# Performance work log

Measured on AMD Instinct MI355X. Metric: run time of the kernel, lower is better.

Reference implementation:

```python
import jax, jax.numpy as jnp
import numpy as np

B, T, D, H = 128, 512, 256, 512


def setup_inputs() -> dict:
    key = jax.random.key(0)
    k1, k2, k3 = jax.random.split(key, 3)
    x = jax.random.normal(k1, (B, T, D), dtype=jnp.float32)
    Wx = jax.random.normal(k2, (D, 4 * H), dtype=jnp.float32) * 0.05
    Wh = jax.random.normal(k3, (H, 4 * H), dtype=jnp.float32) * 0.05
    b = jnp.zeros((4 * H,), dtype=jnp.float32)
    return {"x": x, "Wx": Wx, "Wh": Wh, "b": b}


def reference(x, Wx, Wh, b):
    # DynamicRNN: transpose [B,T,D]->[T,B,D], unroll LSTM cell per timestep,
    # stack outputs, transpose back, return (outputs, final_state).
    xs = jnp.transpose(x, (1, 0, 2))  # [T, B, D]
    Bn = x.shape[0]
    Hn = Wh.shape[0]
    h0 = jnp.zeros((Bn, Hn), dtype=x.dtype)
    c0 = jnp.zeros((Bn, Hn), dtype=x.dtype)

    # Precompute input-side projection for all timesteps (same math, batched).
    zx = jnp.einsum('tbd,dg->tbg', xs, Wx) + b  # [T, B, 4H]

    def step(carry, zx_t):
        h, c = carry
        z = zx_t + h @ Wh  # [B, 4H]
        i, f, g, o = jnp.split(z, 4, axis=-1)
        i = jax.nn.sigmoid(i)
        f = jax.nn.sigmoid(f)
        g = jnp.tanh(g)
        o = jax.nn.sigmoid(o)
        c_new = f * c + i * g
        h_new = o * jnp.tanh(c_new)
        return (h_new, c_new), h_new

    (hT, cT), ys = jax.lax.scan(step, (h0, c0), zx)  # ys: [T, B, H]
    outputs = jnp.transpose(ys, (1, 0, 2))  # [B, T, H]
    return (outputs, hT, cT)
```

## Files before the change

kernel.cpp:

```cpp
#include <hip/hip_runtime.h>
#include <hip/hip_bf16.h>


#define B_   128
#define T_   512
#define D_   256
#define H_   512
#define G4_  2048
#define NBLK 128
#define KH   16
#define KX   8
#define XROW 264

typedef __attribute__((ext_vector_type(8))) short short8;
typedef __attribute__((ext_vector_type(4))) short short4v;
typedef __attribute__((ext_vector_type(4))) float float4v;
typedef __attribute__((ext_vector_type(4))) int   int4v;

__device__ inline unsigned short f2bf_bits(float f) {
    union { float f; unsigned u; } v; v.f = f;
    unsigned r = (v.u + 0x7FFFu + ((v.u >> 16) & 1u)) >> 16;
    return (unsigned short)r;
}

__device__ inline float sigmoid_fast(float x) {
    return 1.f / (1.f + __expf(-x));
}

__device__ inline float tanh_fast(float x) {
    float a = fabsf(x);
    float e = __expf(-2.f * a);
    float r = (1.f - e) / (1.f + e);
    return copysignf(r, x);
}

__device__ inline short4v pack_bf4(float4v v) {
    short4v o;
    o[0] = (short)f2bf_bits(v[0]);
    o[1] = (short)f2bf_bits(v[1]);
    o[2] = (short)f2bf_bits(v[2]);
    o[3] = (short)f2bf_bits(v[3]);
    return o;
}

union HAu { int4v i4; short8 s8; };

__global__ __launch_bounds__(512, 2) void lstm_persistent(
    const float* __restrict__ x, const float* __restrict__ Wx,
    const float* __restrict__ Wh, const float* __restrict__ bias,
    float* __restrict__ out, unsigned short* __restrict__ hbuf,
    unsigned int* __restrict__ flags)
{
    const int tid  = threadIdx.x;
    const int lane = tid & 63;
    const int wave = tid >> 6;
    const int ms   = wave & 3;
    const int nt   = wave >> 2;
    const int ct   = blockIdx.x & 63;
    const int bt   = blockIdx.x >> 6;
    const int jh0  = ct * 8;

    __shared__ float zls[64 * 33];
    __shared__ float cls[64 * 8];
    __shared__ float bls[32];
    __shared__ unsigned short xls[2][64 * XROW];

    for (int i = tid; i < 64 * 8; i += 512) cls[i] = 0.f;
    if (tid < 32) bls[tid] = bias[(tid >> 3) * 512 + jh0 + (tid & 7)];

    const int l15 = lane & 15;
    const int l4  = lane >> 4;
    const int ncol = nt * 16 + l15;
    const int col  = (ncol >> 3) * 512 + jh0 + (ncol & 7);
    short8 wfrag[KX + KH];
#pragma unroll
    for (int ks = 0; ks < KX + KH; ++ks) {
        short8 w;
#pragma unroll
        for (int j = 0; j < 8; ++j) {
            int k = ks * 32 + l4 * 8 + j;
            float v = (k < D_) ? Wx[(size_t)k * G4_ + col]
                               : Wh[(size_t)(k - D_) * G4_ + col];
            w[j] = (short)f2bf_bits(v);
        }
        wfrag[ks] = w;
    }

    const int srow = tid >> 5;
    const int scol = (tid & 31) * 4;
    const float* xbase = x + (size_t)(bt * 64) * (T_ * D_);

    const int mrow = ms * 16 + l15;
    const int gb_a = bt * 64 + mrow;

    const int bl = tid >> 3, ug = tid & 7;
    const int gb_g = bt * 64 + bl;

    unsigned int* myflag = flags + bt * 64 + lane;

    short4v rxp[8];
#pragma unroll
    for (int r = 0; r < 4; ++r) {
        const float* xp = xbase + (size_t)(r * 16 + srow) * (T_ * D_);
        int row = r * 16 + srow;
        *(short4v*)(&xls[0][row * XROW + scol]) =
            pack_bf4(*(const float4v*)(xp + scol));
        *(short4v*)(&xls[0][row * XROW + scol + 128]) =
            pack_bf4(*(const float4v*)(xp + scol + 128));
    }
    __syncthreads();
    float4v accx = {0.f, 0.f, 0.f, 0.f};
#pragma unroll
    for (int ks = 0; ks < KX; ++ks) {
        short8 a = *(const short8*)(&xls[0][mrow * XROW + ks * 32 + l4 * 8]);
        accx = __builtin_amdgcn_mfma_f32_16x16x32_bf16(a, wfrag[ks], accx, 0, 0, 0);
    }
#pragma unroll
    for (int r = 0; r < 4; ++r) {
        const float* xp = xbase + (size_t)(r * 16 + srow) * (T_ * D_) + D_;
        rxp[r * 2]     = pack_bf4(*(const float4v*)(xp + scol));
        rxp[r * 2 + 1] = pack_bf4(*(const float4v*)(xp + scol + 128));
    }

    int cur = 0;
    for (int t = 0; t < T_; ++t) {
        if (t + 1 < T_) {
            unsigned short* xb = xls[(t + 1) & 1];
#pragma unroll
            for (int r = 0; r < 4; ++r) {
                int row = r * 16 + srow;
                *(short4v*)(xb + row * XROW + scol)       = rxp[r * 2];
                *(short4v*)(xb + row * XROW + scol + 128) = rxp[r * 2 + 1];
            }
        }

        if (t) {
            unsigned tgt = (unsigned)t;
            while (true) {
                unsigned f = __hip_atomic_load(myflag, __ATOMIC_RELAXED,
                                               __HIP_MEMORY_SCOPE_AGENT);
                if (__all((int)(f >= tgt))) break;
            }
        }

        HAu ha[KH];
        {
            const unsigned short* hb0 =
                hbuf + ((size_t)(cur * 64 + l4) * 128 + gb_a) * 8;
#pragma unroll
            for (int ks = 0; ks < KH; ++ks) {
                const unsigned short* ap = hb0 + (size_t)ks * (4 * 128 * 8);
                asm volatile("global_load_dwordx4 %0, %1, off sc0 sc1"
                             : "=v"(ha[ks].i4) : "v"(ap));
            }
        }

        float4v a0 = accx;
        float4v a1 = {0.f, 0.f, 0.f, 0.f};
        asm volatile("s_waitcnt vmcnt(8)" ::: "memory");
        __builtin_amdgcn_sched_barrier(0);
#pragma unroll
        for (int ks = 0; ks < 8; ++ks)
            a0 = __builtin_amdgcn_mfma_f32_16x16x32_bf16(
                     ha[ks].s8, wfrag[KX + ks], a0, 0, 0, 0);
        asm volatile("s_waitcnt vmcnt(0)" ::: "memory");
        __builtin_amdgcn_sched_barrier(0);
#pragma unroll
        for (int ks = 8; ks < KH; ++ks)
            a1 = __builtin_amdgcn_mfma_f32_16x16x32_bf16(
                     ha[ks].s8, wfrag[KX + ks], a1, 0, 0, 0);
#pragma unroll
        for (int r = 0; r < 4; ++r) {
            int row = ms * 16 + l4 * 4 + r;
            zls[row * 33 + nt * 16 + l15] = a0[r] + a1[r];
        }
        __syncthreads();

        {
            float zi = zls[bl * 33 + ug]      + bls[ug];
            float zf = zls[bl * 33 + 8 + ug]  + bls[8 + ug];
            float zg = zls[bl * 33 + 16 + ug] + bls[16 + ug];
            float zo = zls[bl * 33 + 24 + ug] + bls[24 + ug];
            float ig = sigmoid_fast(zi);
            float fg = sigmoid_fast(zf);
            float gg = tanh_fast(zg);
            float og = sigmoid_fast(zo);
            float cold = cls[bl * 8 + ug];
            float cnew = fg * cold + ig * gg;
            float hnew = og * tanh_fast(cnew);
            cls[bl * 8 + ug] = cnew;
            unsigned hv = (unsigned)f2bf_bits(hnew);
            unsigned short* hp = hbuf
                + ((size_t)(((t + 1) & 1) * 64 + ct) * 128 + gb_g) * 8 + ug;
            asm volatile("global_store_short %0, %1, off sc0 sc1"
                         :: "v"(hp), "v"(hv) : "memory");
            out[(size_t)gb_g * (T_ * H_) + (size_t)t * H_ + jh0 + ug] = hnew;
            if (t == T_ - 1) {
                const size_t BTH = (size_t)B_ * T_ * H_;
                out[BTH + (size_t)gb_g * H_ + jh0 + ug] = hnew;
                out[BTH + (size_t)B_ * H_ + (size_t)gb_g * H_ + jh0 + ug] = cnew;
            }
        }
        asm volatile("s_waitcnt vmcnt(0)" ::: "memory");
        __syncthreads();

        if (tid == 0)
            __hip_atomic_store(flags + bt * 64 + ct, (unsigned)(t + 1),
                               __ATOMIC_RELAXED, __HIP_MEMORY_SCOPE_AGENT);

        float4v nacc = {0.f, 0.f, 0.f, 0.f};
        if (t + 1 < T_) {
            const unsigned short* xb = xls[(t + 1) & 1];
#pragma unroll
            for (int ks = 0; ks < KX; ++ks) {
                short8 a = *(const short8*)(xb + mrow * XROW + ks * 32 + l4 * 8);
                nacc = __builtin_amdgcn_mfma_f32_16x16x32_bf16(
                           a, wfrag[ks], nacc, 0, 0, 0);
            }
            if (t + 2 < T_) {
#pragma unroll
                for (int r = 0; r < 4; ++r) {
                    const float* xp = xbase + (size_t)(r * 16 + srow) * (T_ * D_)
                                    + (size_t)(t + 2) * D_;
                    rxp[r * 2]     = pack_bf4(*(const float4v*)(xp + scol));
                    rxp[r * 2 + 1] = pack_bf4(*(const float4v*)(xp + scol + 128));
                }
            }
        }
        accx = nacc;
        cur ^= 1;
    }
}

extern "C" void kernel_launch(void* const* d_in, const int* in_sizes, int n_in,
                              void* d_out, int out_size, void* d_ws, size_t ws_size,
                              hipStream_t stream) {
    const float* x    = (const float*)d_in[0];
    const float* Wx   = (const float*)d_in[1];
    const float* Wh   = (const float*)d_in[2];
    const float* bias = (const float*)d_in[3];
    float* out = (float*)d_out;

    unsigned short* hbuf = (unsigned short*)d_ws;
    const size_t hbuf_bytes = (size_t)2 * 64 * 128 * 8 * sizeof(unsigned short);
    unsigned int* flags = (unsigned int*)((char*)d_ws + hbuf_bytes);

    hipMemsetAsync(d_ws, 0, hbuf_bytes + 1024, stream);

    lstm_persistent<<<dim3(NBLK), dim3(512), 0, stream>>>(
        x, Wx, Wh, bias, out, hbuf, flags);
}
```

Baseline: 2.250 ms.

## Replace flag-based grid sync with tagged self-validating hidden-state records

Drops the per-block flag counters and the store-wait-then-flag handshake. Each hidden-state chunk is now written as a 16-byte record carrying the data plus an XOR tag tied to the timestep, and readers spin on the data itself until the tags match. The K-dimension load is also split across the two wave groups, which exchange fragments through LDS, so each wave fetches half the remote h data. This is meant to cut one global round trip per step from the serial recurrence. In exchange it adds tag checks, an extra __syncthreads, more LDS, and relies on 16-byte stores being observed atomically.

```diff
diff --git a/kernel.cpp b/kernel.cpp
--- a/kernel.cpp
+++ b/kernel.cpp
@@ -8,9 +8,10 @@
 #define H_   512
 #define G4_  2048
 #define NBLK 128
-#define KH   16
 #define KX   8
 #define XROW 264
+#define TAGK 0x9E3779B97F4A7C15ull
+#define PLANE_B (128 * 128 * 16)
 
 typedef __attribute__((ext_vector_type(8))) short short8;
 typedef __attribute__((ext_vector_type(4))) short short4v;
@@ -43,13 +44,33 @@
     return o;
 }
 
-union HAu { int4v i4; short8 s8; };
+union Frag { int i[4]; int4v i4; short8 s8; };
+
+#define LOADH(H)                                                             \
+    {                                                                        \
+        _Pragma("unroll")                                                    \
+        for (int k_ = (H) * 4; k_ < (H) * 4 + 4; ++k_) {                     \
+            const char* p_ = cb + k_ * 16384;                                \
+            asm volatile("global_load_dwordx4 %0, %1, off sc0 sc1"           \
+                         : "=v"(rec[2 * k_]) : "v"(p_));                     \
+            asm volatile("global_load_dwordx4 %0, %1, off offset:2048 sc0 sc1" \
+                         : "=v"(rec[2 * k_ + 1]) : "v"(p_));                 \
+        }                                                                    \
+    }
+
+#define VALIDH(H, okv)                                                       \
+    {                                                                        \
+        okv = 1;                                                             \
+        _Pragma("unroll")                                                    \
+        for (int i_ = (H) * 8; i_ < (H) * 8 + 8; ++i_)                       \
+            okv &= (int)((((unsigned)(rec[i_][0] ^ rec[i_][2])) == tagLo) &  \
+                         (((unsigned)(rec[i_][1] ^ rec[i_][3])) == tagHi));  \
+    }
 
 __global__ __launch_bounds__(512, 2) void lstm_persistent(
     const float* __restrict__ x, const float* __restrict__ Wx,
     const float* __restrict__ Wh, const float* __restrict__ bias,
-    float* __restrict__ out, unsigned short* __restrict__ hbuf,
-    unsigned int* __restrict__ flags)
+    float* __restrict__ out, char* __restrict__ hbuf)
 {
     const int tid  = threadIdx.x;
     const int lane = tid & 63;
@@ -63,7 +84,9 @@
     __shared__ float zls[64 * 33];
     __shared__ float cls[64 * 8];
     __shared__ float bls[32];
+    __shared__ __align__(16) unsigned short hls[512];
     __shared__ unsigned short xls[2][64 * XROW];
+    __shared__ int4v exls[4 * 16 * 64];
 
     for (int i = tid; i < 64 * 8; i += 512) cls[i] = 0.f;
     if (tid < 32) bls[tid] = bias[(tid >> 3) * 512 + jh0 + (tid & 7)];
@@ -72,9 +95,9 @@
     const int l4  = lane >> 4;
     const int ncol = nt * 16 + l15;
     const int col  = (ncol >> 3) * 512 + jh0 + (ncol & 7);
-    short8 wfrag[KX + KH];
-#pragma unroll
-    for (int ks = 0; ks < KX + KH; ++ks) {
+    short8 wfrag[KX + 16];
+#pragma unroll
+    for (int ks = 0; ks < KX + 16; ++ks) {
         short8 w;
 #pragma unroll
         for (int j = 0; j < 8; ++j) {
@@ -93,10 +116,13 @@
     const int mrow = ms * 16 + l15;
     const int gb_a = bt * 64 + mrow;
 
+    char* const crb = hbuf + ((size_t)(nt * 64 + l4 * 2) * 128 + gb_a) * 16;
+
     const int bl = tid >> 3, ug = tid & 7;
     const int gb_g = bt * 64 + bl;
 
-    unsigned int* myflag = flags + bt * 64 + lane;
+    char* const prb = hbuf +
+        ((size_t)(ct * 2 + (tid & 1)) * 128 + bt * 64 + (tid >> 1)) * 16;
 
     short4v rxp[8];
 #pragma unroll
@@ -122,7 +148,8 @@
         rxp[r * 2 + 1] = pack_bf4(*(const float4v*)(xp + scol + 128));
     }
 
-    int cur = 0;
+    unsigned long long tcur = 0;
+
     for (int t = 0; t < T_; ++t) {
         if (t + 1 < T_) {
             unsigned short* xb = xls[(t + 1) & 1];
@@ -134,45 +161,70 @@
             }
         }
 
+        float4v zsum = accx;
+
         if (t) {
-            unsigned tgt = (unsigned)t;
-            while (true) {
-                unsigned f = __hip_atomic_load(myflag, __ATOMIC_RELAXED,
-                                               __HIP_MEMORY_SCOPE_AGENT);
-                if (__all((int)(f >= tgt))) break;
-            }
-        }
-
-        HAu ha[KH];
-        {
-            const unsigned short* hb0 =
-                hbuf + ((size_t)(cur * 64 + l4) * 128 + gb_a) * 8;
-#pragma unroll
-            for (int ks = 0; ks < KH; ++ks) {
-                const unsigned short* ap = hb0 + (size_t)ks * (4 * 128 * 8);
-                asm volatile("global_load_dwordx4 %0, %1, off sc0 sc1"
-                             : "=v"(ha[ks].i4) : "v"(ap));
-            }
-        }
-
-        float4v a0 = accx;
-        float4v a1 = {0.f, 0.f, 0.f, 0.f};
-        asm volatile("s_waitcnt vmcnt(8)" ::: "memory");
-        __builtin_amdgcn_sched_barrier(0);
-#pragma unroll
-        for (int ks = 0; ks < 8; ++ks)
-            a0 = __builtin_amdgcn_mfma_f32_16x16x32_bf16(
-                     ha[ks].s8, wfrag[KX + ks], a0, 0, 0, 0);
-        asm volatile("s_waitcnt vmcnt(0)" ::: "memory");
-        __builtin_amdgcn_sched_barrier(0);
-#pragma unroll
-        for (int ks = 8; ks < KH; ++ks)
-            a1 = __builtin_amdgcn_mfma_f32_16x16x32_bf16(
-                     ha[ks].s8, wfrag[KX + ks], a1, 0, 0, 0);
+            const unsigned tagLo = (unsigned)tcur;
+            const unsigned tagHi = (unsigned)(tcur >> 32);
+            const char* cb = crb + (size_t)(t & 1) * PLANE_B;
+            int4v rec[16];
+
+            LOADH(0)
+            LOADH(1)
+
+            asm volatile("s_waitcnt vmcnt(8)" ::: "memory");
+            __builtin_amdgcn_sched_barrier(0);
+            int ok0; VALIDH(0, ok0)
+            while (!__all(ok0)) {
+                LOADH(0)
+                asm volatile("s_waitcnt vmcnt(0)" ::: "memory");
+                __builtin_amdgcn_sched_barrier(0);
+                VALIDH(0, ok0)
+            }
+#pragma unroll
+            for (int k = 0; k < 4; ++k) {
+                Frag f;
+                f.i[0] = rec[2 * k][0];     f.i[1] = rec[2 * k][1];
+                f.i[2] = rec[2 * k + 1][0]; f.i[3] = rec[2 * k + 1][1];
+                exls[(ms * 16 + nt * 8 + k) * 64 + lane] = f.i4;
+                zsum = __builtin_amdgcn_mfma_f32_16x16x32_bf16(
+                           f.s8, wfrag[KX + nt * 8 + k], zsum, 0, 0, 0);
+            }
+
+            asm volatile("s_waitcnt vmcnt(0)" ::: "memory");
+            __builtin_amdgcn_sched_barrier(0);
+            int ok1; VALIDH(1, ok1)
+            while (!__all(ok1)) {
+                LOADH(1)
+                asm volatile("s_waitcnt vmcnt(0)" ::: "memory");
+                __builtin_amdgcn_sched_barrier(0);
+                VALIDH(1, ok1)
+            }
+#pragma unroll
+            for (int k = 4; k < 8; ++k) {
+                Frag f;
+                f.i[0] = rec[2 * k][0];     f.i[1] = rec[2 * k][1];
+                f.i[2] = rec[2 * k + 1][0]; f.i[3] = rec[2 * k + 1][1];
+                exls[(ms * 16 + nt * 8 + k) * 64 + lane] = f.i4;
+                zsum = __builtin_amdgcn_mfma_f32_16x16x32_bf16(
+                           f.s8, wfrag[KX + nt * 8 + k], zsum, 0, 0, 0);
+            }
+
+            __syncthreads();
+
+#pragma unroll
+            for (int k = 0; k < 8; ++k) {
+                Frag f;
+                f.i4 = exls[(ms * 16 + (nt ^ 1) * 8 + k) * 64 + lane];
+                zsum = __builtin_amdgcn_mfma_f32_16x16x32_bf16(
+                           f.s8, wfrag[KX + (nt ^ 1) * 8 + k], zsum, 0, 0, 0);
+            }
+        }
+
 #pragma unroll
         for (int r = 0; r < 4; ++r) {
             int row = ms * 16 + l4 * 4 + r;
-            zls[row * 33 + nt * 16 + l15] = a0[r] + a1[r];
+            zls[row * 33 + nt * 16 + l15] = zsum[r];
         }
         __syncthreads();
 
@@ -189,11 +241,7 @@
             float cnew = fg * cold + ig * gg;
             float hnew = og * tanh_fast(cnew);
             cls[bl * 8 + ug] = cnew;
-            unsigned hv = (unsigned)f2bf_bits(hnew);
-            unsigned short* hp = hbuf
-                + ((size_t)(((t + 1) & 1) * 64 + ct) * 128 + gb_g) * 8 + ug;
-            asm volatile("global_store_short %0, %1, off sc0 sc1"
-                         :: "v"(hp), "v"(hv) : "memory");
+            hls[bl * 8 + ug] = f2bf_bits(hnew);
             out[(size_t)gb_g * (T_ * H_) + (size_t)t * H_ + jh0 + ug] = hnew;
             if (t == T_ - 1) {
                 const size_t BTH = (size_t)B_ * T_ * H_;
@@ -201,12 +249,20 @@
                 out[BTH + (size_t)B_ * H_ + (size_t)gb_g * H_ + jh0 + ug] = cnew;
             }
         }
-        asm volatile("s_waitcnt vmcnt(0)" ::: "memory");
         __syncthreads();
 
-        if (tid == 0)
-            __hip_atomic_store(flags + bt * 64 + ct, (unsigned)(t + 1),
-                               __ATOMIC_RELAXED, __HIP_MEMORY_SCOPE_AGENT);
+        if (t + 1 < T_ && tid < 128) {
+            const int jr = tid & 1, rr = tid >> 1;
+            unsigned long long d =
+                *(const unsigned long long*)(&hls[rr * 8 + jr * 4]);
+            unsigned long long sh = d ^ (tcur + TAGK);
+            int4v st;
+            st[0] = (int)(unsigned)d;  st[1] = (int)(unsigned)(d >> 32);
+            st[2] = (int)(unsigned)sh; st[3] = (int)(unsigned)(sh >> 32);
+            char* p = prb + (size_t)((t + 1) & 1) * PLANE_B;
+            asm volatile("global_store_dwordx4 %0, %1, off sc0 sc1"
+                         :: "v"(p), "v"(st) : "memory");
+        }
 
         float4v nacc = {0.f, 0.f, 0.f, 0.f};
         if (t + 1 < T_) {
@@ -228,7 +284,7 @@
             }
         }
         accx = nacc;
-        cur ^= 1;
+        tcur += TAGK;
     }
 }
 
@@ -241,12 +297,10 @@
     const float* bias = (const float*)d_in[3];
     float* out = (float*)d_out;
 
-    unsigned short* hbuf = (unsigned short*)d_ws;
-    const size_t hbuf_bytes = (size_t)2 * 64 * 128 * 8 * sizeof(unsigned short);
-    unsigned int* flags = (unsigned int*)((char*)d_ws + hbuf_bytes);
-
-    hipMemsetAsync(d_ws, 0, hbuf_bytes + 1024, stream);
+    char* hbuf = (char*)d_ws;
+
+    hipMemsetAsync(d_ws, 0, (size_t)2 * PLANE_B, stream);
 
     lstm_persistent<<<dim3(NBLK), dim3(512), 0, stream>>>(
-        x, Wx, Wh, bias, out, hbuf, flags);
-}
+        x, Wx, Wh, bias, out, hbuf);
+}
```

Measured after the change: 4.255 ms. 89.2% more time.
